# Performance work log

Measured on AMD Instinct MI355X. Metric: run time of the kernel, lower is better.

The kernel has to match this reference:

```python
import jax, jax.numpy as jnp
import numpy as np
from jax import lax

C = 256       # d_model
NH = 8        # nhead
D = C // NH   # head dim
P = 4         # pool_size == pool_size2
EPS_LN = 1e-5
EPS_ATTN = 1e-6


def setup_inputs() -> dict:
    key = jax.random.key(0)
    ks = jax.random.split(key, 8)
    w = lambda k, sh: jax.random.normal(k, sh, jnp.float32) * 0.02
    return {
        "x": jax.random.normal(ks[0], (4, C, 128, 128), jnp.float32),
        "source": jax.random.normal(ks[1], (4, C, 128, 128), jnp.float32),
        "norm1_g": jnp.ones((C,), jnp.float32),
        "norm1_b": jnp.zeros((C,), jnp.float32),
        "w_q": w(ks[2], (C, C)),      # [in, out] layout
        "w_k": w(ks[3], (C, C)),
        "w_v": w(ks[4], (C, C)),
        "w_merge": w(ks[5], (C, C)),
        "mlp_w1": w(ks[6], (2 * C, 2 * C)),
        "mlp_w2": w(ks[7], (2 * C, C)),
        "norm2_g": jnp.ones((C,), jnp.float32),
        "norm2_b": jnp.zeros((C,), jnp.float32),
    }


def layernorm(t, g, b):
    m = t.mean(-1, keepdims=True)
    v = ((t - m) ** 2).mean(-1, keepdims=True)
    return (t - m) * lax.rsqrt(v + EPS_LN) * g + b


def maxpool(t):  # t: [N, C, H, W] -> [N, C, H/P, W/P]
    return lax.reduce_window(t, -jnp.inf, lax.max, (1, 1, P, P), (1, 1, P, P), 'VALID')


def reference(x, source, norm1_g, norm1_b, w_q, w_k, w_v, w_merge,
              mlp_w1, mlp_w2, norm2_g, norm2_b):
    bs, Cc, H1, W1 = x.shape
    # norm_before path: max_pool -> NHWC -> layernorm
    q_in = layernorm(jnp.transpose(maxpool(x), (0, 2, 3, 1)), norm1_g, norm1_b)       # [b,h,w,C]
    s_in = layernorm(jnp.transpose(maxpool(source), (0, 2, 3, 1)), norm1_g, norm1_b)  # [b,h2,w2,C]
    hq, wq = q_in.shape[1], q_in.shape[2]

    Q = (q_in @ w_q).reshape(bs, -1, NH, D)  # [b, L, nh, d]
    K = (s_in @ w_k).reshape(bs, -1, NH, D)  # [b, S, nh, d]
    V = (s_in @ w_v).reshape(bs, -1, NH, D)

    # LinearAttention (LoFTR): elu feature map
    Qp = jax.nn.elu(Q) + 1.0
    Kp = jax.nn.elu(K) + 1.0
    L_kv = V.shape[1]
    Vn = V / L_kv  # numerical-stability scaling as in original
    KV = jnp.einsum('nshd,nshv->nhdv', Kp, Vn)                     # [b,nh,d,d]
    Z = 1.0 / (jnp.einsum('nlhd,nhd->nlh', Qp, Kp.sum(1)) + EPS_ATTN)
    msg = jnp.einsum('nlhd,nhdv,nlh->nlhv', Qp, KV, Z) * L_kv      # [b,L,nh,d]

    msg = msg.reshape(bs, -1, NH * D) @ w_merge                    # merge
    msg = msg.reshape(bs, hq, wq, Cc).transpose(0, 3, 1, 2)        # [b,C,h,w]
    # bilinear upsample scale_factor=P, align_corners=False (half-pixel centers)
    msg = jax.image.resize(msg, (bs, Cc, H1, W1), method='bilinear')

    # MLP on cat([x, message], channel) in NHWC
    cat = jnp.concatenate([x, msg], axis=1).transpose(0, 2, 3, 1)  # [b,H,W,2C]
    m = jax.nn.relu(cat @ mlp_w1) @ mlp_w2                         # [b,H,W,C]
    m = layernorm(m, norm2_g, norm2_b).transpose(0, 3, 1, 2)       # [b,C,H,W]
    return x + m
```

## Files before the change

kernel.cpp:

```cpp
#include <hip/hip_runtime.h>

typedef unsigned short u16;
typedef __bf16 bf16x8 __attribute__((ext_vector_type(8)));
typedef float f32x4 __attribute__((ext_vector_type(4)));
typedef float f32x16 __attribute__((ext_vector_type(16)));

__device__ __forceinline__ u16 f2bf(float f) {
  union { float f; unsigned u; } v; v.f = f;
  unsigned r = (v.u + 0x7FFFu + ((v.u >> 16) & 1u)) >> 16;
  return (u16)r;
}
__device__ __forceinline__ float bf2f(u16 h) {
  union { unsigned u; float f; } v; v.u = ((unsigned)h) << 16;
  return v.f;
}

__device__ __forceinline__ void load_lds16(const void* g, void* l) {
  __builtin_amdgcn_global_load_lds((__attribute__((address_space(1))) void*)(g),
                                   (__attribute__((address_space(3))) void*)(l), 16, 0, 0);
}

__device__ __forceinline__ void gemm128(
    const u16* __restrict__ A, const u16* __restrict__ Bt,
    float* __restrict__ Cf, u16* __restrict__ Cb,
    int N, int K, int mode,
    u16* lA, u16* lB)
{
  const int tid  = threadIdx.x;
  const int wave = tid >> 6;
  const int lane = tid & 63;
  const int wi = wave >> 1, wj = wave & 1;
  const int m0 = blockIdx.x * 128;
  const int n0 = blockIdx.y * 128;
  const int srow = lane >> 2;
  const int skc  = (lane & 3) * 8;
  const int lm = lane & 15;
  const int kq = (lane >> 4) * 8;

  f32x4 acc[4][4];
#pragma unroll
  for (int i = 0; i < 4; ++i)
#pragma unroll
    for (int j = 0; j < 4; ++j)
#pragma unroll
      for (int e = 0; e < 4; ++e) acc[i][j][e] = 0.f;

  const int kTiles = K >> 5;
  for (int kt = 0; kt < kTiles; ++kt) {
    __syncthreads();
#pragma unroll
    for (int t = 0; t < 2; ++t) {
      const int ci = wave * 2 + t;
      const u16* ga = A + (size_t)(m0 + ci * 16 + srow) * K + kt * 32 + skc;
      load_lds16(ga, &lA[ci * 512]);
      const u16* gb = Bt + (size_t)(n0 + ci * 16 + srow) * K + kt * 32 + skc;
      load_lds16(gb, &lB[ci * 512]);
    }
    asm volatile("s_waitcnt vmcnt(0)" ::: "memory");
    __syncthreads();
    bf16x8 af[4], bfr[4];
#pragma unroll
    for (int i = 0; i < 4; ++i)
      af[i] = *(const bf16x8*)&lA[(wi * 64 + i * 16 + lm) * 32 + kq];
#pragma unroll
    for (int j = 0; j < 4; ++j)
      bfr[j] = *(const bf16x8*)&lB[(wj * 64 + j * 16 + lm) * 32 + kq];
#pragma unroll
    for (int i = 0; i < 4; ++i)
#pragma unroll
      for (int j = 0; j < 4; ++j)
        acc[i][j] = __builtin_amdgcn_mfma_f32_16x16x32_bf16(af[i], bfr[j], acc[i][j], 0, 0, 0);
  }

  const int lq = lane >> 4;
#pragma unroll
  for (int i = 0; i < 4; ++i) {
#pragma unroll
    for (int j = 0; j < 4; ++j) {
      const int col  = n0 + wj * 64 + j * 16 + lm;
      const int row0 = m0 + wi * 64 + i * 16 + lq * 4;
#pragma unroll
      for (int r = 0; r < 4; ++r) {
        float v = acc[i][j][r];
        const size_t idx = (size_t)(row0 + r) * N + col;
        if (mode == 1)      Cf[idx] = (v > 0.f) ? (v + 1.f) : __expf(v);
        else if (mode == 2) Cf[idx] = v * (1.f / 1024.f);
        else                Cb[idx] = f2bf(v);
      }
    }
  }
}

__global__ __launch_bounds__(256) void qkv_kernel(
    const u16* __restrict__ qbf, const u16* __restrict__ sbf,
    const u16* __restrict__ wqT, const u16* __restrict__ wkT, const u16* __restrict__ wvT,
    float* __restrict__ Qp, float* __restrict__ Kp, float* __restrict__ Vn)
{
  __shared__ __attribute__((aligned(16))) u16 lA[128 * 32];
  __shared__ __attribute__((aligned(16))) u16 lB[128 * 32];
  const int z = blockIdx.z;
  const u16* A = (z == 0) ? qbf : sbf;
  const u16* B = (z == 0) ? wqT : (z == 1) ? wkT : wvT;
  float* C = (z == 0) ? Qp : (z == 1) ? Kp : Vn;
  gemm128(A, B, C, nullptr, 256, 256, (z == 2) ? 2 : 1, lA, lB);
}

__global__ __launch_bounds__(256) void merge_kernel(
    const u16* __restrict__ msg2, const u16* __restrict__ wmT, u16* __restrict__ merged)
{
  __shared__ __attribute__((aligned(16))) u16 lA[128 * 32];
  __shared__ __attribute__((aligned(16))) u16 lB[128 * 32];
  gemm128(msg2, wmT, nullptr, merged, 256, 256, 3, lA, lB);
}

__global__ __launch_bounds__(256, 2) void mlp1_kernel(
    const u16* __restrict__ xbf, const u16* __restrict__ ub,
    const u16* __restrict__ w1T, u16* __restrict__ hid)
{
  __shared__ __attribute__((aligned(16))) u16 lA[128 * 64];
  __shared__ __attribute__((aligned(16))) u16 lB[256 * 64];
  const int tid = threadIdx.x;
  const int w = tid >> 6, l = tid & 63;
  const int wi = w >> 1, wj = w & 1;
  const int n0 = blockIdx.x * 256;
  const int m0 = blockIdx.y * 128;
  const int sr8 = l >> 3;
  const int kbg = (l & 7) ^ sr8;

  f32x16 acc[2][4];
#pragma unroll
  for (int ti = 0; ti < 2; ++ti)
#pragma unroll
    for (int tj = 0; tj < 4; ++tj)
#pragma unroll
      for (int e = 0; e < 16; ++e) acc[ti][tj][e] = 0.f;

  for (int kc = 0; kc < 8; ++kc) {
    const u16* Asrc = (kc < 4) ? (xbf + kc * 64) : (ub + (kc - 4) * 64);
    __syncthreads();
#pragma unroll
    for (int it = 0; it < 4; ++it) {
      const int r = it * 32 + w * 8 + sr8;
      load_lds16(Asrc + (size_t)(m0 + r) * 256 + kbg * 8, &lA[(it * 32 + w * 8) * 64]);
    }
#pragma unroll
    for (int it = 0; it < 8; ++it) {
      const int r = it * 32 + w * 8 + sr8;
      load_lds16(w1T + (size_t)(n0 + r) * 512 + kc * 64 + kbg * 8, &lB[(it * 32 + w * 8) * 64]);
    }
    asm volatile("s_waitcnt vmcnt(0)" ::: "memory");
    __syncthreads();
    const int h = l >> 5;
#pragma unroll
    for (int s = 0; s < 4; ++s) {
      const int kb = s * 2 + h;
      bf16x8 af[2], bfr[4];
#pragma unroll
      for (int ti = 0; ti < 2; ++ti) {
        const int rt = wi * 64 + ti * 32 + (l & 31);
        af[ti] = *(const bf16x8*)&lA[rt * 64 + (kb ^ (rt & 7)) * 8];
      }
#pragma unroll
      for (int tj = 0; tj < 4; ++tj) {
        const int rn = wj * 128 + tj * 32 + (l & 31);
        bfr[tj] = *(const bf16x8*)&lB[rn * 64 + (kb ^ (rn & 7)) * 8];
      }
#pragma unroll
      for (int ti = 0; ti < 2; ++ti)
#pragma unroll
        for (int tj = 0; tj < 4; ++tj)
          acc[ti][tj] = __builtin_amdgcn_mfma_f32_32x32x16_bf16(af[ti], bfr[tj], acc[ti][tj], 0, 0, 0);
    }
  }

  const int h = l >> 5;
#pragma unroll
  for (int ti = 0; ti < 2; ++ti)
#pragma unroll
    for (int tj = 0; tj < 4; ++tj)
#pragma unroll
      for (int rg = 0; rg < 16; ++rg) {
        const int row = m0 + wi * 64 + ti * 32 + (rg & 3) + 8 * (rg >> 2) + 4 * h;
        const int col = n0 + wj * 128 + tj * 32 + (l & 31);
        const float v = acc[ti][tj][rg];
        hid[(size_t)row * 512 + col] = f2bf(v > 0.f ? v : 0.f);
      }
}

__global__ __launch_bounds__(256, 3) void mlp2_kernel(
    const u16* __restrict__ hid, const u16* __restrict__ w2T,
    const float* __restrict__ x, const float* __restrict__ g,
    const float* __restrict__ bb, float* __restrict__ out, int pixbase)
{
  __shared__ __attribute__((aligned(16))) u16 lds[64 * 64 + 256 * 64];
  __shared__ float redA[64][4];
  __shared__ float redB[64][4];
  __shared__ float statm[64], statr[64];
  u16* lA = lds;
  u16* lB = lds + 64 * 64;
  u16* sm = lds;

  const int tid = threadIdx.x;
  const int w = tid >> 6, l = tid & 63;
  const int m0 = blockIdx.x * 64;
  const int sr8 = l >> 3;
  const int kbg = (l & 7) ^ sr8;

  f32x16 acc[2][2];
#pragma unroll
  for (int ti = 0; ti < 2; ++ti)
#pragma unroll
    for (int tj = 0; tj < 2; ++tj)
#pragma unroll
      for (int e = 0; e < 16; ++e) acc[ti][tj][e] = 0.f;

  for (int kc = 0; kc < 8; ++kc) {
    __syncthreads();
#pragma unroll
    for (int it = 0; it < 2; ++it) {
      const int r = it * 32 + w * 8 + sr8;
      load_lds16(hid + (size_t)(m0 + r) * 512 + kc * 64 + kbg * 8, &lA[(it * 32 + w * 8) * 64]);
    }
#pragma unroll
    for (int it = 0; it < 8; ++it) {
      const int r = it * 32 + w * 8 + sr8;
      load_lds16(w2T + (size_t)r * 512 + kc * 64 + kbg * 8, &lB[(it * 32 + w * 8) * 64]);
    }
    asm volatile("s_waitcnt vmcnt(0)" ::: "memory");
    __syncthreads();
    const int h = l >> 5;
#pragma unroll
    for (int s = 0; s < 4; ++s) {
      const int kb = s * 2 + h;
      bf16x8 af[2], bfr[2];
#pragma unroll
      for (int ti = 0; ti < 2; ++ti) {
        const int rt = ti * 32 + (l & 31);
        af[ti] = *(const bf16x8*)&lA[rt * 64 + (kb ^ (rt & 7)) * 8];
      }
#pragma unroll
      for (int tj = 0; tj < 2; ++tj) {
        const int rn = w * 64 + tj * 32 + (l & 31);
        bfr[tj] = *(const bf16x8*)&lB[rn * 64 + (kb ^ (rn & 7)) * 8];
      }
#pragma unroll
      for (int ti = 0; ti < 2; ++ti)
#pragma unroll
        for (int tj = 0; tj < 2; ++tj)
          acc[ti][tj] = __builtin_amdgcn_mfma_f32_32x32x16_bf16(af[ti], bfr[tj], acc[ti][tj], 0, 0, 0);
    }
  }

  __syncthreads();
  {
    const int h = l >> 5;
#pragma unroll
    for (int ti = 0; ti < 2; ++ti)
#pragma unroll
      for (int tj = 0; tj < 2; ++tj)
#pragma unroll
        for (int rg = 0; rg < 16; ++rg) {
          const int prow = ti * 32 + (rg & 3) + 8 * (rg >> 2) + 4 * h;
          const int pcol = w * 64 + tj * 32 + (l & 31);
          sm[prow * 258 + pcol] = f2bf(acc[ti][tj][rg]);
        }
  }
  __syncthreads();
  {
    const int p = tid & 63, q = tid >> 6;
    float s = 0.f, s2 = 0.f;
    for (int k = 0; k < 64; ++k) {
      const float v = bf2f(sm[p * 258 + q * 64 + k]);
      s += v; s2 += v * v;
    }
    redA[p][q] = s; redB[p][q] = s2;
  }
  __syncthreads();
  if (tid < 64) {
    const float ss = redA[tid][0] + redA[tid][1] + redA[tid][2] + redA[tid][3];
    const float qq = redB[tid][0] + redB[tid][1] + redB[tid][2] + redB[tid][3];
    const float mean = ss * (1.f / 256.f);
    const float var = qq * (1.f / 256.f) - mean * mean;
    statm[tid] = mean;
    statr[tid] = rsqrtf(var + 1e-5f);
  }
  __syncthreads();
  {
    const int gp = pixbase + m0;
    const int b = gp >> 14;
    const int rem = gp & 16383;
    const int i = rem >> 7;
    const int j0 = rem & 127;
    const int p = tid & 63, cg = tid >> 6;
    const int j = j0 + p;
    const float mu = statm[p], rs = statr[p];
    for (int k = 0; k < 64; ++k) {
      const int c = cg * 64 + k;
      const float v = (bf2f(sm[p * 258 + c]) - mu) * rs * g[c] + bb[c];
      const size_t oi = (((size_t)b * 256 + c) * 128 + i) * 128 + j;
      out[oi] = x[oi] + v;
    }
  }
}

__global__ __launch_bounds__(256) void transpose_w_kernel(
    const float* __restrict__ wq, const float* __restrict__ wk,
    const float* __restrict__ wv, const float* __restrict__ wm,
    const float* __restrict__ w1, const float* __restrict__ w2,
    u16* __restrict__ oq, u16* __restrict__ okk, u16* __restrict__ ov,
    u16* __restrict__ om, u16* __restrict__ o1, u16* __restrict__ o2)
{
  __shared__ float ts[64][65];
  int bid = blockIdx.x;
  const float* src; u16* dst; int K, N, t;
  if (bid < 64) {
    int wsel = bid >> 4; t = bid & 15; K = 256; N = 256;
    src = wsel == 0 ? wq : wsel == 1 ? wk : wsel == 2 ? wv : wm;
    dst = wsel == 0 ? oq : wsel == 1 ? okk : wsel == 2 ? ov : om;
  } else if (bid < 128) { t = bid - 64; K = 512; N = 512; src = w1; dst = o1; }
  else                  { t = bid - 128; K = 512; N = 256; src = w2; dst = o2; }
  const int ntn = N >> 6;
  const int tn = t % ntn, tk = t / ntn;
  const int tid = threadIdx.x, ln = tid & 63, lrr = tid >> 6;
  for (int k = 0; k < 64; k += 4)
    ts[k + lrr][ln] = src[(size_t)(tk * 64 + k + lrr) * N + tn * 64 + ln];
  __syncthreads();
  for (int k = 0; k < 64; k += 4)
    dst[(size_t)(tn * 64 + k + lrr) * K + tk * 64 + ln] = f2bf(ts[ln][k + lrr]);
}

__global__ __launch_bounds__(256) void pool_ln_kernel(
    const float* __restrict__ x, const float* __restrict__ src,
    const float* __restrict__ g, const float* __restrict__ bb,
    u16* __restrict__ qout, u16* __restrict__ sout)
{
  __shared__ float pool[256 * 33];
  __shared__ float redA[8][32];
  __shared__ float redB[8][32];
  __shared__ float stat_m[32];
  __shared__ float stat_r[32];
  const int ph = blockIdx.x, b = blockIdx.y;
  const float* in = blockIdx.z ? src : x;
  u16* out = blockIdx.z ? sout : qout;
  const int tid = threadIdx.x;
  const int pw = tid & 31, cg = tid >> 5;
  for (int kk = 0; kk < 32; ++kk) {
    const int c = cg * 32 + kk;
    const float* base = in + (((size_t)b * 256 + c) * 128 + ph * 4) * 128 + pw * 4;
    float4 v0 = *(const float4*)(base);
    float4 v1 = *(const float4*)(base + 128);
    float4 v2 = *(const float4*)(base + 256);
    float4 v3 = *(const float4*)(base + 384);
    float m = fmaxf(fmaxf(fmaxf(v0.x, v0.y), fmaxf(v0.z, v0.w)),
                    fmaxf(fmaxf(v1.x, v1.y), fmaxf(v1.z, v1.w)));
    m = fmaxf(m, fmaxf(fmaxf(v2.x, v2.y), fmaxf(v2.z, v2.w)));
    m = fmaxf(m, fmaxf(fmaxf(v3.x, v3.y), fmaxf(v3.z, v3.w)));
    pool[c * 33 + pw] = m;
  }
  __syncthreads();
  float s = 0.f, s2 = 0.f;
  for (int i = 0; i < 32; ++i) {
    float v = pool[(cg * 32 + i) * 33 + pw];
    s += v; s2 += v * v;
  }
  redA[cg][pw] = s; redB[cg][pw] = s2;
  __syncthreads();
  if (tid < 32) {
    float ss = 0.f, ss2 = 0.f;
    for (int i = 0; i < 8; ++i) { ss += redA[i][tid]; ss2 += redB[i][tid]; }
    float mean = ss * (1.f / 256.f);
    float var = ss2 * (1.f / 256.f) - mean * mean;
    stat_m[tid] = mean;
    stat_r[tid] = rsqrtf(var + 1e-5f);
  }
  __syncthreads();
  const float gc = g[tid], bc = bb[tid];
  const size_t rowbase = ((size_t)b * 1024 + ph * 32) * 256;
  for (int p = 0; p < 32; ++p) {
    float v = (pool[tid * 33 + p] - stat_m[p]) * stat_r[p] * gc + bc;
    out[rowbase + (size_t)p * 256 + tid] = f2bf(v);
  }
}

__global__ __launch_bounds__(256) void kv_kernel(
    const float* __restrict__ Kp, const float* __restrict__ Vn,
    float* __restrict__ kvbuf)
{
  __shared__ float kch[128 * 33];
  __shared__ float vch[128 * 33];
  const int h = blockIdx.x, b = blockIdx.y;
  const int tid = threadIdx.x;
  const int d = tid & 31, sl = tid >> 5;
  const int v = tid & 31, dp = tid >> 5;
  float a0 = 0.f, a1 = 0.f, a2 = 0.f, a3 = 0.f, ks = 0.f;
  for (int ch = 0; ch < 8; ++ch) {
    __syncthreads();
    for (int ss = 0; ss < 16; ++ss) {
      const int srow = ch * 128 + ss * 8 + sl;
      const size_t gi = ((size_t)b * 1024 + srow) * 256 + h * 32 + d;
      kch[(ss * 8 + sl) * 33 + d] = Kp[gi];
      vch[(ss * 8 + sl) * 33 + d] = Vn[gi];
    }
    __syncthreads();
    for (int s = 0; s < 128; ++s) {
      const float vv = vch[s * 33 + v];
      a0 += kch[s * 33 + dp] * vv;
      a1 += kch[s * 33 + dp + 8] * vv;
      a2 += kch[s * 33 + dp + 16] * vv;
      a3 += kch[s * 33 + dp + 24] * vv;
    }
    if (tid < 32)
      for (int s = 0; s < 128; ++s) ks += kch[s * 33 + tid];
  }
  float* outp = kvbuf + ((size_t)b * 8 + h) * 1056;
  outp[(dp) * 32 + v]      = a0;
  outp[(dp + 8) * 32 + v]  = a1;
  outp[(dp + 16) * 32 + v] = a2;
  outp[(dp + 24) * 32 + v] = a3;
  if (tid < 32) outp[1024 + tid] = ks;
}

__global__ __launch_bounds__(256) void msg_kernel(
    const float* __restrict__ Qp, const float* __restrict__ kvbuf,
    u16* __restrict__ msg2)
{
  __shared__ float kv[32 * 33];
  __shared__ float ksum[32];
  __shared__ float qch[8 * 33];
  const int lc = blockIdx.x, h = blockIdx.y, b = blockIdx.z;
  const int tid = threadIdx.x;
  const float* kvp = kvbuf + ((size_t)b * 8 + h) * 1056;
  for (int i = tid; i < 1024; i += 256) kv[(i >> 5) * 33 + (i & 31)] = kvp[i];
  if (tid < 32) ksum[tid] = kvp[1024 + tid];
  const int d = tid & 31, lr = tid >> 5;
  const int v = tid & 31;
  for (int ps = 0; ps < 8; ++ps) {
    __syncthreads();
    const int l = lc * 64 + ps * 8 + lr;
    qch[lr * 33 + d] = Qp[((size_t)b * 1024 + l) * 256 + h * 32 + d];
    __syncthreads();
    float dot = 0.f, zden = 0.f;
    for (int dd = 0; dd < 32; ++dd) {
      const float q = qch[lr * 33 + dd];
      dot  += q * kv[dd * 33 + v];
      zden += q * ksum[dd];
    }
    const float m = dot * (1024.f / (zden + 1e-6f));
    msg2[((size_t)b * 1024 + l) * 256 + h * 32 + v] = f2bf(m);
  }
}

__global__ __launch_bounds__(256) void prep_kernel(
    const float* __restrict__ x, const u16* __restrict__ merged,
    u16* __restrict__ xbf, u16* __restrict__ ub, int b0)
{
  __shared__ float ts[64][65];
  const int jc = blockIdx.x, y = blockIdx.y, iz = blockIdx.z;
  const int localb = iz >> 7;
  const int b = b0 + localb;
  const int i = iz & 127;
  const int tid = threadIdx.x;
  if (y < 4) {
    const int cc = y, ln = tid & 63, lrr = tid >> 6;
    const float* xp = x + (size_t)b * 256 * 16384;
    for (int k = 0; k < 64; k += 4)
      ts[k + lrr][ln] = xp[((size_t)(cc * 64 + k + lrr) * 128 + i) * 128 + jc * 64 + ln];
    __syncthreads();
    for (int k = 0; k < 64; k += 4) {
      const size_t row = (size_t)localb * 16384 + (size_t)i * 128 + jc * 64 + k + lrr;
      xbf[row * 256 + cc * 64 + ln] = f2bf(ts[ln][k + lrr]);
    }
  } else {
    const float sy = 0.25f * i - 0.375f;
    const float fy = floorf(sy);
    const float wy = sy - fy;
    const int y0 = max(0, min(31, (int)fy));
    const int y1 = max(0, min(31, (int)fy + 1));
    const u16* mb = merged + (size_t)b * 1024 * 256;
    for (int p = 0; p < 64; ++p) {
      const int j = jc * 64 + p;
      const float sx = 0.25f * j - 0.375f;
      const float fx = floorf(sx);
      const float wx = sx - fx;
      const int x0 = max(0, min(31, (int)fx));
      const int x1 = max(0, min(31, (int)fx + 1));
      const u16* r00 = mb + ((size_t)y0 * 32 + x0) * 256;
      const u16* r01 = mb + ((size_t)y0 * 32 + x1) * 256;
      const u16* r10 = mb + ((size_t)y1 * 32 + x0) * 256;
      const u16* r11 = mb + ((size_t)y1 * 32 + x1) * 256;
      const float v = (1.f - wy) * ((1.f - wx) * bf2f(r00[tid]) + wx * bf2f(r01[tid]))
                    +        wy  * ((1.f - wx) * bf2f(r10[tid]) + wx * bf2f(r11[tid]));
      const size_t row = (size_t)localb * 16384 + (size_t)i * 128 + j;
      ub[row * 256 + tid] = f2bf(v);
    }
  }
}

extern "C" void kernel_launch(void* const* d_in, const int* in_sizes, int n_in,
                              void* d_out, int out_size, void* d_ws, size_t ws_size,
                              hipStream_t stream) {
  (void)in_sizes; (void)n_in; (void)out_size;
  const float* x   = (const float*)d_in[0];
  const float* src = (const float*)d_in[1];
  const float* n1g = (const float*)d_in[2];
  const float* n1b = (const float*)d_in[3];
  const float* w_q = (const float*)d_in[4];
  const float* w_k = (const float*)d_in[5];
  const float* w_v = (const float*)d_in[6];
  const float* w_m = (const float*)d_in[7];
  const float* w1  = (const float*)d_in[8];
  const float* w2  = (const float*)d_in[9];
  const float* n2g = (const float*)d_in[10];
  const float* n2b = (const float*)d_in[11];
  float* out = (float*)d_out;

  char* ws = (char*)d_ws;
  size_t off = 0;
  auto alloc = [&](size_t bytes) -> void* {
    void* p = ws + off;
    off = (off + bytes + 255) & ~(size_t)255;
    return p;
  };
  u16* wqT = (u16*)alloc(256 * 256 * 2);
  u16* wkT = (u16*)alloc(256 * 256 * 2);
  u16* wvT = (u16*)alloc(256 * 256 * 2);
  u16* wmT = (u16*)alloc(256 * 256 * 2);
  u16* w1T = (u16*)alloc(512 * 512 * 2);
  u16* w2T = (u16*)alloc(256 * 512 * 2);
  u16* qbf = (u16*)alloc((size_t)4096 * 256 * 2);
  u16* sbf = (u16*)alloc((size_t)4096 * 256 * 2);
  float* Qp = (float*)alloc((size_t)4096 * 256 * 4);
  float* Kp = (float*)alloc((size_t)4096 * 256 * 4);
  float* Vn = (float*)alloc((size_t)4096 * 256 * 4);
  float* kvb = (float*)alloc((size_t)32 * 1056 * 4);
  u16* msg2   = (u16*)alloc((size_t)4096 * 256 * 2);
  u16* merged = (u16*)alloc((size_t)4096 * 256 * 2);

  size_t remain = (ws_size > off) ? ws_size - off : 0;
  auto need = [](int nb) { return (size_t)nb * 16384 * (256 + 256 + 512) * 2 + 4096; };
  int nb = (remain >= need(4)) ? 4 : (remain >= need(2)) ? 2 : 1;
  u16* xbf = (u16*)alloc((size_t)nb * 16384 * 256 * 2);
  u16* ub  = (u16*)alloc((size_t)nb * 16384 * 256 * 2);
  u16* hid = (u16*)alloc((size_t)nb * 16384 * 512 * 2);

  transpose_w_kernel<<<dim3(160), dim3(256), 0, stream>>>(
      w_q, w_k, w_v, w_m, w1, w2, wqT, wkT, wvT, wmT, w1T, w2T);

  pool_ln_kernel<<<dim3(32, 4, 2), dim3(256), 0, stream>>>(
      x, src, n1g, n1b, qbf, sbf);

  qkv_kernel<<<dim3(32, 2, 3), dim3(256), 0, stream>>>(
      qbf, sbf, wqT, wkT, wvT, Qp, Kp, Vn);

  kv_kernel<<<dim3(8, 4), dim3(256), 0, stream>>>(Kp, Vn, kvb);
  msg_kernel<<<dim3(16, 8, 4), dim3(256), 0, stream>>>(Qp, kvb, msg2);

  merge_kernel<<<dim3(32, 2), dim3(256), 0, stream>>>(msg2, wmT, merged);

  for (int b0 = 0; b0 < 4; b0 += nb) {
    prep_kernel<<<dim3(2, 5, 128 * nb), dim3(256), 0, stream>>>(
        x, merged, xbf, ub, b0);
    mlp1_kernel<<<dim3(2, nb * 128), dim3(256), 0, stream>>>(
        xbf, ub, w1T, hid);
    mlp2_kernel<<<dim3(nb * 256), dim3(256), 0, stream>>>(
        hid, w2T, x, n2g, n2b, out, b0 * 16384);
  }
}
```

Before: 375.2 us.

## Restructure mlp2 as channel-major tile with register LayerNorm epilogue

The second MLP GEMM now computes a transposed tile, with output channels as M and 128 pixels as N, so each block covers a full image row of 128 pixels. LayerNorm statistics are reduced directly from the accumulator registers using a cross-lane shuffle and a small LDS exchange. This replaces the bf16 round-trip through shared memory and the serial per-pixel reduction loops. The final store is now coalesced along pixels in NCHW, and the launch uses half as many blocks with lower occupancy (launch bounds 2 instead of 3) and a larger accumulator footprint.

```diff
diff --git a/kernel.cpp b/kernel.cpp
--- a/kernel.cpp
+++ b/kernel.cpp
@@ -187,120 +187,126 @@
       }
 }
 
-__global__ __launch_bounds__(256, 3) void mlp2_kernel(
+__global__ __launch_bounds__(256, 2) void mlp2_kernel(
     const u16* __restrict__ hid, const u16* __restrict__ w2T,
     const float* __restrict__ x, const float* __restrict__ g,
     const float* __restrict__ bb, float* __restrict__ out, int pixbase)
 {
-  __shared__ __attribute__((aligned(16))) u16 lds[64 * 64 + 256 * 64];
-  __shared__ float redA[64][4];
-  __shared__ float redB[64][4];
-  __shared__ float statm[64], statr[64];
-  u16* lA = lds;
-  u16* lB = lds + 64 * 64;
-  u16* sm = lds;
+  __shared__ __attribute__((aligned(16))) u16 lA[256 * 64];
+  __shared__ __attribute__((aligned(16))) u16 lB[128 * 64];
+  float* sb = (float*)lB;
 
   const int tid = threadIdx.x;
   const int w = tid >> 6, l = tid & 63;
-  const int m0 = blockIdx.x * 64;
+  const int l31 = l & 31, hsel = l >> 5;
+  const int s7 = l31 & 7;
+  const int m0 = blockIdx.x * 128;
   const int sr8 = l >> 3;
   const int kbg = (l & 7) ^ sr8;
 
-  f32x16 acc[2][2];
-#pragma unroll
-  for (int ti = 0; ti < 2; ++ti)
-#pragma unroll
-    for (int tj = 0; tj < 2; ++tj)
-#pragma unroll
-      for (int e = 0; e < 16; ++e) acc[ti][tj][e] = 0.f;
+  f32x16 acc[2][4];
+#pragma unroll
+  for (int mi = 0; mi < 2; ++mi)
+#pragma unroll
+    for (int nj = 0; nj < 4; ++nj)
+#pragma unroll
+      for (int e = 0; e < 16; ++e) acc[mi][nj][e] = 0.f;
 
   for (int kc = 0; kc < 8; ++kc) {
     __syncthreads();
-#pragma unroll
-    for (int it = 0; it < 2; ++it) {
-      const int r = it * 32 + w * 8 + sr8;
-      load_lds16(hid + (size_t)(m0 + r) * 512 + kc * 64 + kbg * 8, &lA[(it * 32 + w * 8) * 64]);
-    }
 #pragma unroll
     for (int it = 0; it < 8; ++it) {
       const int r = it * 32 + w * 8 + sr8;
-      load_lds16(w2T + (size_t)r * 512 + kc * 64 + kbg * 8, &lB[(it * 32 + w * 8) * 64]);
+      load_lds16(w2T + (size_t)r * 512 + kc * 64 + kbg * 8, &lA[(it * 32 + w * 8) * 64]);
+    }
+#pragma unroll
+    for (int it = 0; it < 4; ++it) {
+      const int r = it * 32 + w * 8 + sr8;
+      load_lds16(hid + (size_t)(m0 + r) * 512 + kc * 64 + kbg * 8, &lB[(it * 32 + w * 8) * 64]);
     }
     asm volatile("s_waitcnt vmcnt(0)" ::: "memory");
     __syncthreads();
-    const int h = l >> 5;
 #pragma unroll
     for (int s = 0; s < 4; ++s) {
-      const int kb = s * 2 + h;
-      bf16x8 af[2], bfr[2];
-#pragma unroll
-      for (int ti = 0; ti < 2; ++ti) {
-        const int rt = ti * 32 + (l & 31);
-        af[ti] = *(const bf16x8*)&lA[rt * 64 + (kb ^ (rt & 7)) * 8];
-      }
-#pragma unroll
-      for (int tj = 0; tj < 2; ++tj) {
-        const int rn = w * 64 + tj * 32 + (l & 31);
-        bfr[tj] = *(const bf16x8*)&lB[rn * 64 + (kb ^ (rn & 7)) * 8];
-      }
-#pragma unroll
-      for (int ti = 0; ti < 2; ++ti)
-#pragma unroll
-        for (int tj = 0; tj < 2; ++tj)
-          acc[ti][tj] = __builtin_amdgcn_mfma_f32_32x32x16_bf16(af[ti], bfr[tj], acc[ti][tj], 0, 0, 0);
-    }
-  }
-
-  __syncthreads();
-  {
-    const int h = l >> 5;
-#pragma unroll
-    for (int ti = 0; ti < 2; ++ti)
-#pragma unroll
-      for (int tj = 0; tj < 2; ++tj)
-#pragma unroll
-        for (int rg = 0; rg < 16; ++rg) {
-          const int prow = ti * 32 + (rg & 3) + 8 * (rg >> 2) + 4 * h;
-          const int pcol = w * 64 + tj * 32 + (l & 31);
-          sm[prow * 258 + pcol] = f2bf(acc[ti][tj][rg]);
-        }
-  }
-  __syncthreads();
-  {
-    const int p = tid & 63, q = tid >> 6;
-    float s = 0.f, s2 = 0.f;
-    for (int k = 0; k < 64; ++k) {
-      const float v = bf2f(sm[p * 258 + q * 64 + k]);
-      s += v; s2 += v * v;
-    }
-    redA[p][q] = s; redB[p][q] = s2;
-  }
-  __syncthreads();
-  if (tid < 64) {
-    const float ss = redA[tid][0] + redA[tid][1] + redA[tid][2] + redA[tid][3];
-    const float qq = redB[tid][0] + redB[tid][1] + redB[tid][2] + redB[tid][3];
-    const float mean = ss * (1.f / 256.f);
-    const float var = qq * (1.f / 256.f) - mean * mean;
-    statm[tid] = mean;
-    statr[tid] = rsqrtf(var + 1e-5f);
-  }
-  __syncthreads();
-  {
-    const int gp = pixbase + m0;
-    const int b = gp >> 14;
-    const int rem = gp & 16383;
-    const int i = rem >> 7;
-    const int j0 = rem & 127;
-    const int p = tid & 63, cg = tid >> 6;
-    const int j = j0 + p;
-    const float mu = statm[p], rs = statr[p];
-    for (int k = 0; k < 64; ++k) {
-      const int c = cg * 64 + k;
-      const float v = (bf2f(sm[p * 258 + c]) - mu) * rs * g[c] + bb[c];
-      const size_t oi = (((size_t)b * 256 + c) * 128 + i) * 128 + j;
-      out[oi] = x[oi] + v;
-    }
-  }
+      const int kb = s * 2 + hsel;
+      bf16x8 af[2], bf[4];
+#pragma unroll
+      for (int mi = 0; mi < 2; ++mi) {
+        const int rt = w * 64 + mi * 32 + l31;
+        af[mi] = *(const bf16x8*)&lA[rt * 64 + ((kb ^ s7) << 3)];
+      }
+#pragma unroll
+      for (int nj = 0; nj < 4; ++nj) {
+        const int rn = nj * 32 + l31;
+        bf[nj] = *(const bf16x8*)&lB[rn * 64 + ((kb ^ s7) << 3)];
+      }
+#pragma unroll
+      for (int mi = 0; mi < 2; ++mi)
+#pragma unroll
+        for (int nj = 0; nj < 4; ++nj)
+          acc[mi][nj] = __builtin_amdgcn_mfma_f32_32x32x16_bf16(af[mi], bf[nj], acc[mi][nj], 0, 0, 0);
+    }
+  }
+
+  float S[4], Q[4];
+#pragma unroll
+  for (int nj = 0; nj < 4; ++nj) {
+    float s = 0.f, q = 0.f;
+#pragma unroll
+    for (int mi = 0; mi < 2; ++mi)
+#pragma unroll
+      for (int rg = 0; rg < 16; ++rg) {
+        const float v = acc[mi][nj][rg];
+        s += v; q += v * v;
+      }
+    s += __shfl_xor(s, 32, 64);
+    q += __shfl_xor(q, 32, 64);
+    S[nj] = s; Q[nj] = q;
+  }
+  __syncthreads();
+  if (hsel == 0) {
+#pragma unroll
+    for (int nj = 0; nj < 4; ++nj) {
+      sb[w * 128 + nj * 32 + l31]       = S[nj];
+      sb[512 + w * 128 + nj * 32 + l31] = Q[nj];
+    }
+  }
+  __syncthreads();
+  if (tid < 128) {
+    const float Sf = sb[tid] + sb[128 + tid] + sb[256 + tid] + sb[384 + tid];
+    const float Qf = sb[512 + tid] + sb[640 + tid] + sb[768 + tid] + sb[896 + tid];
+    const float mean = Sf * (1.f / 256.f);
+    const float var = Qf * (1.f / 256.f) - mean * mean;
+    sb[1024 + tid] = mean;
+    sb[1152 + tid] = rsqrtf(var + 1e-5f);
+  }
+  __syncthreads();
+
+  float mu[4], rs[4];
+#pragma unroll
+  for (int nj = 0; nj < 4; ++nj) {
+    mu[nj] = sb[1024 + nj * 32 + l31];
+    rs[nj] = sb[1152 + nj * 32 + l31];
+  }
+
+  const int gp = pixbase + m0;
+  const int b = gp >> 14;
+  const int i = (gp & 16383) >> 7;
+
+#pragma unroll
+  for (int mi = 0; mi < 2; ++mi)
+#pragma unroll
+    for (int rg = 0; rg < 16; ++rg) {
+      const int ch = w * 64 + mi * 32 + (rg & 3) + 8 * (rg >> 2) + 4 * hsel;
+      const float gg = g[ch], bv = bb[ch];
+      const size_t base = ((size_t)(b * 256 + ch) * 128 + i) * 128;
+#pragma unroll
+      for (int nj = 0; nj < 4; ++nj) {
+        const int p = nj * 32 + l31;
+        const float v = (acc[mi][nj][rg] - mu[nj]) * rs[nj] * gg + bv;
+        out[base + p] = x[base + p] + v;
+      }
+    }
 }
 
 __global__ __launch_bounds__(256) void transpose_w_kernel(
@@ -562,7 +568,7 @@
         x, merged, xbf, ub, b0);
     mlp1_kernel<<<dim3(2, nb * 128), dim3(256), 0, stream>>>(
         xbf, ub, w1T, hid);
-    mlp2_kernel<<<dim3(nb * 256), dim3(256), 0, stream>>>(
+    mlp2_kernel<<<dim3(nb * 128), dim3(256), 0, stream>>>(
         hid, w2T, x, n2g, n2b, out, b0 * 16384);
   }
 }
```

New measurement: 365.2 us. -2.7%, faster.
